# Kernel tuning notes

Hardware: AMD Instinct MI355X
Metric: run time of the kernel (lower is better)

## Reference

```python
import jax, jax.numpy as jnp
import numpy as np
import math

NL = 2
ENC = 64

def _ln(x, g, b):
    m = x.mean(-1, keepdims=True)
    v = ((x - m) ** 2).mean(-1, keepdims=True)
    return (x - m) * jax.lax.rsqrt(v + 1e-5) * g + b

def _sinu(vals):
    half = ENC // 2
    freq = jnp.exp(jnp.arange(half, dtype=vals.dtype) * (-math.log(10000.0) / half))
    a = vals[..., None] * freq
    return jnp.concatenate([jnp.sin(a), jnp.cos(a)], -1)

def _ssm(x, ng, nb, piw, pib, pw, pb, ig, ib):
    # SSMBlock with LinearAttention core: x + proj_out(LN(silu(z)*sigmoid(gate)))
    h = _ln(x, ng, nb)
    zi = h @ piw + pib
    z, gate = jnp.split(zi, 2, axis=-1)
    u = _ln(jax.nn.silu(z) * jax.nn.sigmoid(gate), ig, ib)
    return x + u @ pw + pb

def _fwd(s, attn_maps, km, se_w1, se_b1, se_w2, se_b2,
         f_ng, f_nb, f_piw, f_pib, f_pow, f_pob, f_ig, f_ib,
         b_ng, b_nb, b_piw, b_pib, b_pow, b_pob, b_ig, b_ib,
         mrg_w, mrg_b, nrm_g, nrm_b,
         ffn_ng, ffn_nb, ffn_w1, ffn_b1, ffn_w2, ffn_b2, H, W):
    B, K, D = s.shape
    w = attn_maps / (attn_maps.sum(-1, keepdims=True) + 1e-8)  # [B,K,N]
    gy = jnp.arange(H, dtype=s.dtype) / max(H - 1, 1)
    gx = jnp.arange(W, dtype=s.dtype) / max(W - 1, 1)
    grid_y = jnp.repeat(gy, W)  # [N], meshgrid-ij flattened
    grid_x = jnp.tile(gx, H)
    cy = (w * grid_y).sum(-1)  # [B,K]
    cx = (w * grid_x).sum(-1)
    spread = jnp.sqrt((w * ((grid_y - cy[..., None]) ** 2 + (grid_x - cx[..., None]) ** 2)).sum(-1))
    enc = jnp.concatenate([_sinu(cy), _sinu(cx), spread[..., None]], -1)  # [B,K,129]
    s = s + jax.nn.gelu(enc @ se_w1 + se_b1, approximate=False) @ se_w2 + se_b2
    # spatial order: identical every layer since attn_maps is fixed
    order = jnp.argsort(cy * W + cx, axis=-1)  # [B,K]
    rv = jnp.argsort(order, axis=-1)           # inverse permutation
    for i in range(NL):
        r = s
        so = jnp.take_along_axis(s, order[..., None], axis=1)
        f = _ssm(so, f_ng[i], f_nb[i], f_piw[i], f_pib[i], f_pow[i], f_pob[i], f_ig[i], f_ib[i])
        bb = jnp.flip(_ssm(jnp.flip(so, 1), b_ng[i], b_nb[i], b_piw[i], b_pib[i], b_pow[i], b_pob[i], b_ig[i], b_ib[i]), 1)
        m = jnp.concatenate([f, bb], -1) @ mrg_w[i] + mrg_b[i]
        s = _ln(r + jnp.take_along_axis(m, rv[..., None], axis=1), nrm_g[i], nrm_b[i])
        h = _ln(s, ffn_ng[i], ffn_nb[i])
        s = s + jax.nn.gelu(h @ ffn_w1[i] + ffn_b1[i], approximate=False) @ ffn_w2[i] + ffn_b2[i]
        s = s * km[..., None]
    return s

def setup_inputs() -> dict:
    B, K, D, DI, H, W = 32, 256, 512, 1024, 64, 64
    N = H * W
    ks = iter(jax.random.split(jax.random.key(0), 64))
    def g(shape, sc=0.02):
        return jax.random.normal(next(ks), shape, dtype=jnp.float32) * sc
    inp = {
        's': jax.random.normal(next(ks), (B, K, D), dtype=jnp.float32),
        'attn_maps': jax.random.uniform(next(ks), (B, K, N), dtype=jnp.float32),
        'km': jnp.ones((B, K), jnp.float32),
        'se_w1': g((2 * ENC + 1, D)), 'se_b1': jnp.zeros((D,), jnp.float32),
        'se_w2': g((D, D)), 'se_b2': jnp.zeros((D,), jnp.float32),
    }
    for p in ('f', 'b'):
        inp[p + '_ng'] = jnp.ones((NL, D), jnp.float32)
        inp[p + '_nb'] = jnp.zeros((NL, D), jnp.float32)
        inp[p + '_piw'] = g((NL, D, 2 * DI))
        inp[p + '_pib'] = jnp.zeros((NL, 2 * DI), jnp.float32)
        inp[p + '_pow'] = g((NL, DI, D))
        inp[p + '_pob'] = jnp.zeros((NL, D), jnp.float32)
        inp[p + '_ig'] = jnp.ones((NL, DI), jnp.float32)
        inp[p + '_ib'] = jnp.zeros((NL, DI), jnp.float32)
    inp['mrg_w'] = g((NL, 2 * D, D)); inp['mrg_b'] = jnp.zeros((NL, D), jnp.float32)
    inp['nrm_g'] = jnp.ones((NL, D), jnp.float32); inp['nrm_b'] = jnp.zeros((NL, D), jnp.float32)
    inp['ffn_ng'] = jnp.ones((NL, D), jnp.float32); inp['ffn_nb'] = jnp.zeros((NL, D), jnp.float32)
    inp['ffn_w1'] = g((NL, D, 4 * D)); inp['ffn_b1'] = jnp.zeros((NL, 4 * D), jnp.float32)
    inp['ffn_w2'] = g((NL, 4 * D, D)); inp['ffn_b2'] = jnp.zeros((NL, D), jnp.float32)
    inp['H'] = H
    inp['W'] = W
    return inp

def reference(s, attn_maps, km, se_w1, se_b1, se_w2, se_b2,
              f_ng, f_nb, f_piw, f_pib, f_pow, f_pob, f_ig, f_ib,
              b_ng, b_nb, b_piw, b_pib, b_pow, b_pob, b_ig, b_ib,
              mrg_w, mrg_b, nrm_g, nrm_b,
              ffn_ng, ffn_nb, ffn_w1, ffn_b1, ffn_w2, ffn_b2, H, W):
    return _fwd(s, attn_maps, km, se_w1, se_b1, se_w2, se_b2,
                f_ng, f_nb, f_piw, f_pib, f_pow, f_pob, f_ig, f_ib,
                b_ng, b_nb, b_piw, b_pib, b_pow, b_pob, b_ig, b_ib,
                mrg_w, mrg_b, nrm_g, nrm_b,
                ffn_ng, ffn_nb, ffn_w1, ffn_b1, ffn_w2, ffn_b2, H, W)
```

## Files before the change

### kernel.cpp

```cpp
#include <hip/hip_runtime.h>
#include <cstdint>
#include <cstddef>


typedef unsigned short u16;
typedef __bf16 bf16x8 __attribute__((ext_vector_type(8)));
typedef float f32x4 __attribute__((ext_vector_type(4)));

#define MROWS 8192

__device__ __forceinline__ u16 f2bf(float f){
  unsigned u = __float_as_uint(f);
  u += 0x7FFFu + ((u >> 16) & 1u);
  return (u16)(u >> 16);
}
__device__ __forceinline__ float bf2f(u16 v){
  return __uint_as_float((unsigned)v << 16);
}

__device__ __forceinline__ float wred64(float v){
#pragma unroll
  for (int o = 32; o > 0; o >>= 1) v += __shfl_xor(v, o, 64);
  return v;
}

#define GLD16(gp, lp) __builtin_amdgcn_global_load_lds( \
    (const __attribute__((address_space(1))) unsigned int*)(gp), \
    (__attribute__((address_space(3))) unsigned int*)(lp), 16, 0, 0)

struct TDesc { const float* src; u16* dst; int R, Kpad, C, zgate, nbx, base; };
struct TPack { TDesc d[16]; };

__global__ __launch_bounds__(256) void transpose_all(TPack p){
  int bid = blockIdx.x;
  TDesc dd = p.d[0];
#pragma unroll
  for (int i = 1; i < 16; ++i) if (bid >= p.d[i].base) dd = p.d[i];
  int lb = bid - dd.base;
  int bx = lb % dd.nbx, by = lb / dd.nbx;

  __shared__ float tile[32][33];
  int n0 = bx << 5, k0 = by << 5;
  int tx = threadIdx.x & 31, ty = threadIdx.x >> 5;
#pragma unroll
  for (int i = 0; i < 32; i += 8){
    int k = k0 + ty + i, n = n0 + tx;
    int oc = n;
    if (dd.zgate){ int g = n >> 5, sl = n & 31;
      oc = (sl < 16) ? (g << 4) + sl : (dd.C >> 1) + (g << 4) + sl - 16; }
    tile[ty + i][tx] = (k < dd.R) ? dd.src[(size_t)k * dd.C + oc] : 0.f;
  }
  __syncthreads();
#pragma unroll
  for (int i = 0; i < 32; i += 8){
    int n = n0 + ty + i, k = k0 + tx;
    dd.dst[(size_t)n * dd.Kpad + k] = f2bf(tile[tx][ty + i]);
  }
}

__global__ __launch_bounds__(256) void stats_enc(
    const float* __restrict__ attn, u16* __restrict__ enc){
  int row = blockIdx.x;
  const float4* a4 = (const float4*)(attn + (size_t)row * 4096);
  int t = threadIdx.x;
  const float inv63 = 1.0f / 63.0f;
  float s0 = 0, sy = 0, sx = 0, sy2 = 0, sx2 = 0;
#pragma unroll
  for (int i = 0; i < 4; ++i){
    int c = t + 256 * i;
    float4 v = a4[c];
    int n = 4 * c;
#pragma unroll
    for (int e = 0; e < 4; ++e){
      float av = (&v.x)[e];
      int nn = n + e;
      float gy = (float)(nn >> 6) * inv63;
      float gx = (float)(nn & 63) * inv63;
      s0 += av; sy += av * gy; sx += av * gx;
      sy2 += av * gy * gy; sx2 += av * gx * gx;
    }
  }
  s0 = wred64(s0); sy = wred64(sy); sx = wred64(sx);
  sy2 = wred64(sy2); sx2 = wred64(sx2);
  __shared__ float red[4][5];
  __shared__ float outv[3];
  int wv = t >> 6, lane = t & 63;
  if (lane == 0){ red[wv][0]=s0; red[wv][1]=sy; red[wv][2]=sx; red[wv][3]=sy2; red[wv][4]=sx2; }
  __syncthreads();
  if (t == 0){
    float S=0, Ay=0, Ax=0, Ay2=0, Ax2=0;
    for (int w = 0; w < 4; ++w){ S+=red[w][0]; Ay+=red[w][1]; Ax+=red[w][2]; Ay2+=red[w][3]; Ax2+=red[w][4]; }
    float denom = S + 1e-8f;
    float cy = Ay / denom, cx = Ax / denom;
    float sp2 = (Ay2 - 2.f*cy*Ay + cy*cy*S + Ax2 - 2.f*cx*Ax + cx*cx*S) / denom;
    outv[0] = cy; outv[1] = cx; outv[2] = sqrtf(fmaxf(sp2, 0.f));
  }
  __syncthreads();
  if (t < 192){
    float cy = outv[0], cx = outv[1];
    float val = 0.f;
    if (t < 128){
      int j = t & 31;
      float fr = expf(-0.28782313662425572f * (float)j);
      float base = (t < 64) ? cy : cx;
      float ang = base * fr;
      val = ((t >> 5) & 1) ? cosf(ang) : sinf(ang);
    } else if (t == 128) val = outv[2];
    enc[(size_t)row * 192 + t] = f2bf(val);
  }
}

__global__ __launch_bounds__(256) void ln_dual(
    const float* __restrict__ x,
    const float* __restrict__ g1, const float* __restrict__ b1,
    const float* __restrict__ g2, const float* __restrict__ b2,
    u16* __restrict__ o1, u16* __restrict__ o2){
  int row = blockIdx.x * 4 + (threadIdx.x >> 6);
  int lane = threadIdx.x & 63, c = lane * 8;
  const float* xr = x + (size_t)row * 512 + c;
  float v[8];
  *(float4*)(v) = *(const float4*)(xr); *(float4*)(v+4) = *(const float4*)(xr+4);
  float s = 0.f;
#pragma unroll
  for (int j = 0; j < 8; ++j) s += v[j];
  float m = wred64(s) * (1.f/512.f);
  float q = 0.f;
#pragma unroll
  for (int j = 0; j < 8; ++j){ float d = v[j]-m; q += d*d; }
  float rstd = rsqrtf(wred64(q)*(1.f/512.f) + 1e-5f);
  float G1[8],B1[8],G2[8],B2[8];
  *(float4*)(G1)=*(const float4*)(g1+c); *(float4*)(G1+4)=*(const float4*)(g1+c+4);
  *(float4*)(B1)=*(const float4*)(b1+c); *(float4*)(B1+4)=*(const float4*)(b1+c+4);
  *(float4*)(G2)=*(const float4*)(g2+c); *(float4*)(G2+4)=*(const float4*)(g2+c+4);
  *(float4*)(B2)=*(const float4*)(b2+c); *(float4*)(B2+4)=*(const float4*)(b2+c+4);
  u16 u1[8] __attribute__((aligned(16)));
  u16 u2[8] __attribute__((aligned(16)));
#pragma unroll
  for (int j = 0; j < 8; ++j){
    float nv = (v[j]-m)*rstd;
    u1[j] = f2bf(nv*G1[j]+B1[j]);
    u2[j] = f2bf(nv*G2[j]+B2[j]);
  }
  *(uint4*)(o1 + (size_t)row*512 + c) = *(const uint4*)u1;
  *(uint4*)(o2 + (size_t)row*512 + c) = *(const uint4*)u2;
}

__global__ __launch_bounds__(256) void ln1024(
    const u16* __restrict__ x,
    const float* __restrict__ gf, const float* __restrict__ bfp,
    const float* __restrict__ gb, const float* __restrict__ bbp,
    u16* __restrict__ o){
  int row = blockIdx.x * 4 + (threadIdx.x >> 6);
  int lane = threadIdx.x & 63, c = lane * 16;
  const float* g = (row >> 13) ? gb : gf;
  const float* b = (row >> 13) ? bbp : bfp;
  const u16* xr = x + (size_t)row * 1024 + c;
  u16 raw[16] __attribute__((aligned(16)));
  *(uint4*)(raw)     = *(const uint4*)(xr);
  *(uint4*)(raw + 8) = *(const uint4*)(xr + 8);
  float v[16];
#pragma unroll
  for (int j = 0; j < 16; ++j) v[j] = bf2f(raw[j]);
  float s = 0.f;
#pragma unroll
  for (int j = 0; j < 16; ++j) s += v[j];
  float m = wred64(s) * (1.f/1024.f);
  float q = 0.f;
#pragma unroll
  for (int j = 0; j < 16; ++j){ float d = v[j]-m; q += d*d; }
  float rstd = rsqrtf(wred64(q)*(1.f/1024.f) + 1e-5f);
  float G[16], B[16];
#pragma unroll
  for (int i = 0; i < 4; ++i){
    *(float4*)(G + 4*i) = *(const float4*)(g + c + 4*i);
    *(float4*)(B + 4*i) = *(const float4*)(b + c + 4*i);
  }
  u16 u[16] __attribute__((aligned(16)));
#pragma unroll
  for (int j = 0; j < 16; ++j) u[j] = f2bf((v[j]-m)*rstd*G[j] + B[j]);
  *(uint4*)(o + (size_t)row*1024 + c)     = *(const uint4*)(u);
  *(uint4*)(o + (size_t)row*1024 + c + 8) = *(const uint4*)(u + 8);
}

__global__ __launch_bounds__(256) void ln_double(
    const u16* __restrict__ x,
    const float* __restrict__ ng, const float* __restrict__ nb,
    const float* __restrict__ fg, const float* __restrict__ fbv,
    u16* __restrict__ s1, u16* __restrict__ h2){
  int row = blockIdx.x * 4 + (threadIdx.x >> 6);
  int lane = threadIdx.x & 63, c = lane * 8;
  const u16* xr = x + (size_t)row * 512 + c;
  u16 raw[8] __attribute__((aligned(16)));
  *(uint4*)(raw) = *(const uint4*)(xr);
  float v[8];
#pragma unroll
  for (int j = 0; j < 8; ++j) v[j] = bf2f(raw[j]);
  float s = 0.f;
#pragma unroll
  for (int j = 0; j < 8; ++j) s += v[j];
  float m = wred64(s) * (1.f/512.f);
  float q = 0.f;
#pragma unroll
  for (int j = 0; j < 8; ++j){ float d = v[j]-m; q += d*d; }
  float rstd = rsqrtf(wred64(q)*(1.f/512.f) + 1e-5f);
  float NG[8],NB[8],FG[8],FB[8];
  *(float4*)(NG)=*(const float4*)(ng+c); *(float4*)(NG+4)=*(const float4*)(ng+c+4);
  *(float4*)(NB)=*(const float4*)(nb+c); *(float4*)(NB+4)=*(const float4*)(nb+c+4);
  *(float4*)(FG)=*(const float4*)(fg+c); *(float4*)(FG+4)=*(const float4*)(fg+c+4);
  *(float4*)(FB)=*(const float4*)(fbv+c);*(float4*)(FB+4)=*(const float4*)(fbv+c+4);
  float w[8];
#pragma unroll
  for (int j = 0; j < 8; ++j) w[j] = (v[j]-m)*rstd*NG[j] + NB[j];
  u16 us[8] __attribute__((aligned(16)));
#pragma unroll
  for (int j = 0; j < 8; ++j) us[j] = f2bf(w[j]);
  *(uint4*)(s1 + (size_t)row*512 + c) = *(const uint4*)us;
  float s2 = 0.f;
#pragma unroll
  for (int j = 0; j < 8; ++j) s2 += w[j];
  float m2 = wred64(s2) * (1.f/512.f);
  float q2 = 0.f;
#pragma unroll
  for (int j = 0; j < 8; ++j){ float d = w[j]-m2; q2 += d*d; }
  float rstd2 = rsqrtf(wred64(q2)*(1.f/512.f) + 1e-5f);
  u16 u[8] __attribute__((aligned(16)));
#pragma unroll
  for (int j = 0; j < 8; ++j) u[j] = f2bf((w[j]-m2)*rstd2*FG[j] + FB[j]);
  *(uint4*)(h2 + (size_t)row*512 + c) = *(const uint4*)u;
}

template<int EPI, int BM>
__global__ __launch_bounds__(256, (BM == 64) ? 4 : 2) void gemm_bt(
    const u16* __restrict__ A,
    const u16* __restrict__ BT0, const u16* __restrict__ BT1,
    const float* __restrict__ bias0, const float* __restrict__ bias1,
    const void* __restrict__ res,
    float* __restrict__ outF, u16* __restrict__ outB,
    const float* __restrict__ km,
    int K, int N, int ldo){
  constexpr int MR = BM / 32;
  __shared__ u16 Asm[BM * 64];
  __shared__ u16 Bsm[128 * 64];
  const int tid = threadIdx.x, wv = tid >> 6, lane = tid & 63;
  const int m0 = blockIdx.y * BM, n0 = blockIdx.x << 7;
  const int wr = wv >> 1, wc = wv & 1;
  const u16* BT = (m0 < MROWS) ? BT0 : BT1;
  const float* bias = (m0 < MROWS) ? bias0 : bias1;

  const int rowin = lane >> 3;
  const int ksrc = ((16 * (lane & 7)) ^ (rowin << 4)) >> 1;
  const int rA = wv * (BM / 4) + rowin;
  const int rB = (wv << 5) + rowin;
  const u16* gA = A + (size_t)(m0 + rA) * K + ksrc;
  const u16* gB = BT + (size_t)(n0 + rB) * K + ksrc;
  u16* ldsA = Asm + wv * (BM / 4) * 64;
  u16* ldsB = Bsm + (wv << 11);

  f32x4 acc[MR][4] = {};
  const int cbase = 16 * (lane >> 4);
  const int swz = (lane & 7) << 4;

  for (int kt = 0; kt < K; kt += 64){
#pragma unroll
    for (int it = 0; it < BM / 32; ++it)
      GLD16(gA + (size_t)it * 8 * K + kt, ldsA + it * 512);
#pragma unroll
    for (int it = 0; it < 4; ++it)
      GLD16(gB + (size_t)it * 8 * K + kt, ldsB + it * 512);
    __syncthreads();
#pragma unroll
    for (int ks = 0; ks < 64; ks += 32){
      const int cs = ((2 * ks + cbase) ^ swz) >> 1;
      bf16x8 af[MR], bfr[4];
#pragma unroll
      for (int m = 0; m < MR; ++m)
        af[m] = *reinterpret_cast<const bf16x8*>(&Asm[(wr*(BM/2) + m*16 + (lane & 15)) * 64 + cs]);
#pragma unroll
      for (int n = 0; n < 4; ++n)
        bfr[n] = *reinterpret_cast<const bf16x8*>(&Bsm[(wc*64 + n*16 + (lane & 15)) * 64 + cs]);
#pragma unroll
      for (int m = 0; m < MR; ++m)
#pragma unroll
        for (int n = 0; n < 4; ++n)
          acc[m][n] = __builtin_amdgcn_mfma_f32_16x16x32_bf16(af[m], bfr[n], acc[m][n], 0, 0, 0);
    }
    __syncthreads();
  }

  const int lr = (lane >> 4) << 2, lc = lane & 15;
#pragma unroll
  for (int m = 0; m < MR; ++m){
    const int grow0 = m0 + wr * (BM/2) + m * 16 + lr;
    if constexpr (EPI == 3){
#pragma unroll
      for (int n = 0; n < 4; n += 2){
        const int zc = n0 + wc * 64 + n * 16 + lc;
        const int bi = ((zc >> 5) << 4) + lc;
        const float bz = bias[bi], bg = bias[(N >> 1) + bi];
        const int ucol = ((n0 + wc * 64) >> 1) + (n << 3) + lc;
#pragma unroll
        for (int r = 0; r < 4; ++r){
          float z = acc[m][n][r] + bz;
          float g = acc[m][n + 1][r] + bg;
          outB[(size_t)(grow0 + r) * ldo + ucol] =
              f2bf((z / (1.f + expf(-z))) * (1.f / (1.f + expf(-g))));
        }
      }
    } else {
#pragma unroll
      for (int n = 0; n < 4; ++n){
        const int col = n0 + wc * 64 + n * 16 + lc;
        const float bv = bias[col];
#pragma unroll
        for (int r = 0; r < 4; ++r){
          const int grow = grow0 + r;
          float v = acc[m][n][r] + bv;
          if constexpr (EPI == 0){
            outB[(size_t)grow * ldo + col] = f2bf(0.5f * v * (1.f + erff(v * 0.70710678118654752f)));
          } else if constexpr (EPI == 1){
            outF[(size_t)grow * ldo + col] = v + ((const float*)res)[(size_t)grow * N + col];
          } else if constexpr (EPI == 2){
            outF[(size_t)grow * ldo + col] =
                (v + bf2f(((const u16*)res)[(size_t)grow * N + col])) * km[grow];
          } else {
            const int rowout = grow & (MROWS - 1);
            const int coloff = (grow >> 13) << 9;
            outB[(size_t)rowout * ldo + coloff + col] =
                f2bf(v + ((const float*)res)[(size_t)rowout * N + col]);
          }
        }
      }
    }
  }
}

extern "C" void kernel_launch(void* const* d_in, const int* in_sizes, int n_in,
                              void* d_out, int out_size, void* d_ws, size_t ws_size,
                              hipStream_t stream){
  (void)in_sizes; (void)n_in; (void)out_size; (void)ws_size;
  const float* s_in   = (const float*)d_in[0];
  const float* attn   = (const float*)d_in[1];
  const float* km     = (const float*)d_in[2];
  const float* se_w1  = (const float*)d_in[3];
  const float* se_b1  = (const float*)d_in[4];
  const float* se_w2  = (const float*)d_in[5];
  const float* se_b2  = (const float*)d_in[6];
  const float* png[2] = {(const float*)d_in[7],  (const float*)d_in[15]};
  const float* pnb[2] = {(const float*)d_in[8],  (const float*)d_in[16]};
  const float* ppiw[2]= {(const float*)d_in[9],  (const float*)d_in[17]};
  const float* ppib[2]= {(const float*)d_in[10], (const float*)d_in[18]};
  const float* ppow[2]= {(const float*)d_in[11], (const float*)d_in[19]};
  const float* ppob[2]= {(const float*)d_in[12], (const float*)d_in[20]};
  const float* pig[2] = {(const float*)d_in[13], (const float*)d_in[21]};
  const float* pibt[2]= {(const float*)d_in[14], (const float*)d_in[22]};
  const float* mrg_w  = (const float*)d_in[23];
  const float* mrg_b  = (const float*)d_in[24];
  const float* nrm_g  = (const float*)d_in[25];
  const float* nrm_b  = (const float*)d_in[26];
  const float* ffn_ng = (const float*)d_in[27];
  const float* ffn_nb = (const float*)d_in[28];
  const float* ffn_w1 = (const float*)d_in[29];
  const float* ffn_b1 = (const float*)d_in[30];
  const float* ffn_w2 = (const float*)d_in[31];
  const float* ffn_b2 = (const float*)d_in[32];
  float* out = (float*)d_out;

  char* ws = (char*)d_ws;
  size_t off = 0;
  auto alloc = [&](size_t bytes)->char*{
    char* p = ws + off; off += (bytes + 255) & ~(size_t)255; return p; };

  u16* w_sew1 = (u16*)alloc(512 * 192 * 2);
  u16* w_sew2 = (u16*)alloc(512 * 512 * 2);
  u16* w_piw[2][2]; u16* w_pow[2][2];
  for (int d = 0; d < 2; ++d)
    for (int i = 0; i < 2; ++i){
      w_piw[d][i] = (u16*)alloc(2048 * 512 * 2);
      w_pow[d][i] = (u16*)alloc(512 * 1024 * 2);
    }
  u16* w_mrg[2]; u16* w_ffn1[2]; u16* w_ffn2[2];
  for (int i = 0; i < 2; ++i){
    w_mrg[i]  = (u16*)alloc(512 * 1024 * 2);
    w_ffn1[i] = (u16*)alloc(2048 * 512 * 2);
    w_ffn2[i] = (u16*)alloc(512 * 2048 * 2);
  }
  u16*   enc  = (u16*)alloc((size_t)MROWS * 192 * 2);
  u16*   t1h2 = (u16*)alloc((size_t)MROWS * 512 * 2);
  float* sc   = (float*)alloc((size_t)MROWS * 512 * 4);
  u16*   hcat = (u16*)alloc((size_t)2 * MROWS * 512 * 2);
  char*  big  = alloc((size_t)MROWS * 2048 * 2);
  u16*   upre = (u16*)big;
  u16*   r2   = (u16*)big;
  u16*   t2   = (u16*)big;
  u16*   ubf  = (u16*)alloc((size_t)2 * MROWS * 1024 * 2);
  u16*   fbuf = (u16*)alloc((size_t)MROWS * 1024 * 2);
  u16*   s1   = (u16*)alloc((size_t)MROWS * 512 * 2);

  TPack pk; int base = 0, di = 0;
  auto push = [&](const float* src, u16* dst, int R, int Kpad, int C, int zg){
    TDesc& t = pk.d[di++];
    t.src = src; t.dst = dst; t.R = R; t.Kpad = Kpad; t.C = C; t.zgate = zg;
    t.nbx = C / 32; t.base = base;
    base += (C / 32) * (Kpad / 32);
  };
  push(se_w1, w_sew1, 129, 192, 512, 0);
  push(se_w2, w_sew2, 512, 512, 512, 0);
  for (int d = 0; d < 2; ++d)
    for (int i = 0; i < 2; ++i){
      push(ppiw[d] + (size_t)i*512*2048, w_piw[d][i], 512, 512, 2048, 1);
      push(ppow[d] + (size_t)i*1024*512, w_pow[d][i], 1024, 1024, 512, 0);
    }
  for (int i = 0; i < 2; ++i){
    push(mrg_w  + (size_t)i*1024*512, w_mrg[i],  1024, 1024, 512, 0);
    push(ffn_w1 + (size_t)i*512*2048, w_ffn1[i], 512, 512, 2048, 0);
    push(ffn_w2 + (size_t)i*2048*512, w_ffn2[i], 2048, 2048, 512, 0);
  }
  transpose_all<<<base, 256, 0, stream>>>(pk);

  stats_enc<<<MROWS, 256, 0, stream>>>(attn, enc);
  gemm_bt<0,64><<<dim3(4, 128), 256, 0, stream>>>(enc, w_sew1, w_sew1, se_b1, se_b1,
      nullptr, nullptr, t1h2, nullptr, 192, 512, 512);
  gemm_bt<1,64><<<dim3(4, 128), 256, 0, stream>>>(t1h2, w_sew2, w_sew2, se_b2, se_b2,
      s_in, sc, nullptr, nullptr, 512, 512, 512);

  for (int i = 0; i < 2; ++i){
    ln_dual<<<MROWS/4, 256, 0, stream>>>(sc, png[0]+i*512, pnb[0]+i*512,
        png[1]+i*512, pnb[1]+i*512, hcat, hcat + (size_t)MROWS*512);
    gemm_bt<3,128><<<dim3(16, 128), 256, 0, stream>>>(hcat,
        w_piw[0][i], w_piw[1][i], ppib[0]+(size_t)i*2048, ppib[1]+(size_t)i*2048,
        nullptr, nullptr, upre, nullptr, 512, 2048, 1024);
    ln1024<<<(2*MROWS)/4, 256, 0, stream>>>(upre,
        pig[0]+i*1024, pibt[0]+i*1024, pig[1]+i*1024, pibt[1]+i*1024, ubf);
    gemm_bt<4,64><<<dim3(4, 256), 256, 0, stream>>>(ubf,
        w_pow[0][i], w_pow[1][i], ppob[0]+i*512, ppob[1]+i*512,
        sc, nullptr, fbuf, nullptr, 1024, 512, 1024);
    gemm_bt<4,64><<<dim3(4, 128), 256, 0, stream>>>(fbuf,
        w_mrg[i], w_mrg[i], mrg_b+i*512, mrg_b+i*512,
        sc, nullptr, r2, nullptr, 1024, 512, 512);
    ln_double<<<MROWS/4, 256, 0, stream>>>(r2, nrm_g+i*512, nrm_b+i*512,
        ffn_ng+i*512, ffn_nb+i*512, s1, t1h2);
    gemm_bt<0,128><<<dim3(16, 64), 256, 0, stream>>>(t1h2,
        w_ffn1[i], w_ffn1[i], ffn_b1+i*2048, ffn_b1+i*2048,
        nullptr, nullptr, t2, nullptr, 512, 2048, 2048);
    gemm_bt<2,64><<<dim3(4, 128), 256, 0, stream>>>(t2,
        w_ffn2[i], w_ffn2[i], ffn_b2+i*512, ffn_b2+i*512,
        s1, (i == 1 ? out : sc), nullptr, km, 2048, 512, 512);
  }
}
```

Before: 751.9 us.

## Add 256x256 tile GEMM with phased LDS double-buffering for wide projections

Adds a new gemm256 kernel that uses 512 threads, 256x256 output tiles, 128KB of swizzled LDS with two buffers, and an interleaved schedule. In that schedule, global-to-LDS loads for the next K tiles are issued between MFMA phases, with explicit waitcnt, barriers and setprio. It replaces the gemm_bt calls for the SSM input projection (gate epilogue) and the FFN first layer (GELU epilogue). Blocks are remapped in groups of eight to improve L2 locality. The goal is more data reuse per tile and better overlap of memory traffic with matrix cores, at the cost of a single workgroup per CU and fewer blocks (256 for FFN1).

```diff
diff --git a/kernel.cpp b/kernel.cpp
--- a/kernel.cpp
+++ b/kernel.cpp
@@ -27,6 +27,11 @@
 #define GLD16(gp, lp) __builtin_amdgcn_global_load_lds( \
     (const __attribute__((address_space(1))) unsigned int*)(gp), \
     (__attribute__((address_space(3))) unsigned int*)(lp), 16, 0, 0)
+
+#define BARRIER() do { asm volatile("" ::: "memory"); \
+  __builtin_amdgcn_s_barrier(); asm volatile("" ::: "memory"); } while(0)
+#define VMW(n) asm volatile("s_waitcnt vmcnt(" #n ")" ::: "memory")
+#define LGKM0() asm volatile("s_waitcnt lgkmcnt(0)" ::: "memory")
 
 struct TDesc { const float* src; u16* dst; int R, Kpad, C, zgate, nbx, base; };
 struct TPack { TDesc d[16]; };
@@ -291,13 +296,163 @@
 #pragma unroll
   for (int m = 0; m < MR; ++m){
     const int grow0 = m0 + wr * (BM/2) + m * 16 + lr;
+#pragma unroll
+    for (int n = 0; n < 4; ++n){
+      const int col = n0 + wc * 64 + n * 16 + lc;
+      const float bv = bias[col];
+#pragma unroll
+      for (int r = 0; r < 4; ++r){
+        const int grow = grow0 + r;
+        float v = acc[m][n][r] + bv;
+        if constexpr (EPI == 0){
+          outB[(size_t)grow * ldo + col] = f2bf(0.5f * v * (1.f + erff(v * 0.70710678118654752f)));
+        } else if constexpr (EPI == 1){
+          outF[(size_t)grow * ldo + col] = v + ((const float*)res)[(size_t)grow * N + col];
+        } else if constexpr (EPI == 2){
+          outF[(size_t)grow * ldo + col] =
+              (v + bf2f(((const u16*)res)[(size_t)grow * N + col])) * km[grow];
+        } else {
+          const int rowout = grow & (MROWS - 1);
+          const int coloff = (grow >> 13) << 9;
+          outB[(size_t)rowout * ldo + coloff + col] =
+              f2bf(v + ((const float*)res)[(size_t)rowout * N + col]);
+        }
+      }
+    }
+  }
+}
+
+template<int EPI>
+__global__ __launch_bounds__(512, 1) void gemm256(
+    const u16* __restrict__ A,
+    const u16* __restrict__ BT0, const u16* __restrict__ BT1,
+    const float* __restrict__ bias0, const float* __restrict__ bias1,
+    u16* __restrict__ outB, int K, int N, int ldo, int nwg){
+  extern __shared__ u16 lds[];
+  const int tid = threadIdx.x, w = tid >> 6, lane = tid & 63;
+  int bid = (blockIdx.x & 7) * (nwg >> 3) + (blockIdx.x >> 3);
+  const int nbx = N >> 8;
+  const int m0 = (bid / nbx) << 8, n0 = (bid % nbx) << 8;
+  const u16* BT = (m0 < MROWS) ? BT0 : BT1;
+  const float* bias = (m0 < MROWS) ? bias0 : bias1;
+  const int wm = w >> 2, wn = w & 3;
+
+  const int srow = (w << 3) + (lane >> 3);
+  const int scol = ((16 * (lane & 7)) ^ (((lane >> 3) & 7) << 4)) >> 1;
+  const u16* gA = A + (size_t)(m0 + srow) * K + scol;
+  const u16* gB = BT + (size_t)(n0 + srow) * K + scol;
+  const int dstw = (w << 3) * 64;
+
+  auto stA = [&](int b, int h, int kt){
+    const u16* s = gA + (size_t)(h << 7) * K + (kt << 6);
+    u16* d = &lds[((b << 1) + 0) * 16384 + (h << 7) * 64 + dstw];
+    GLD16(s, d); GLD16(s + (size_t)64 * K, d + 64 * 64);
+  };
+  auto stB = [&](int b, int h, int kt){
+    const u16* s = gB + (size_t)(h << 7) * K + (kt << 6);
+    u16* d = &lds[((b << 1) + 1) * 16384 + (h << 7) * 64 + dstw];
+    GLD16(s, d); GLD16(s + (size_t)64 * K, d + 64 * 64);
+  };
+
+  const int swz = (lane & 7) << 4;
+  const int cb = (lane >> 4) << 4;
+  const int fr = lane & 15;
+  auto ldA = [&](int b, int mf, int ks)->bf16x8 {
+    int row = (wm << 7) + (mf << 4) + fr;
+    int byte = ((ks << 6) + cb) ^ swz;
+    return *reinterpret_cast<const bf16x8*>(&lds[((b << 1) + 0) * 16384 + row * 64 + (byte >> 1)]);
+  };
+  auto ldB = [&](int b, int nf, int ks)->bf16x8 {
+    int row = (wn << 6) + (nf << 4) + fr;
+    int byte = ((ks << 6) + cb) ^ swz;
+    return *reinterpret_cast<const bf16x8*>(&lds[((b << 1) + 1) * 16384 + row * 64 + (byte >> 1)]);
+  };
+
+  f32x4 acc[8][4] = {};
+  bf16x8 aA[8], bB[2][4];
+  const int nt2 = K >> 7;
+
+  stA(0,0,0); stA(0,1,0); stB(0,0,0); stB(0,1,0);
+  stB(1,0,1); stB(1,1,1);
+  VMW(4);
+  BARRIER();
+
+#pragma unroll 1
+  for (int j = 0; j < nt2; ++j){
+    const int kt1 = 2*j + 1;
+    const bool more = (j + 1 < nt2);
+    const int ktn0 = 2*j + 2, ktn1 = 2*j + 3;
+
+#define PHASE_MFMA(MB, BH)                                              \
+    BARRIER(); LGKM0();                                                 \
+    __builtin_amdgcn_s_setprio(1);                                      \
+    _Pragma("unroll")                                                   \
+    for (int m = 0; m < 4; ++m)                                         \
+      _Pragma("unroll")                                                 \
+      for (int n = 0; n < 2; ++n){                                      \
+        acc[(MB)*4+m][(BH)*2+n] = __builtin_amdgcn_mfma_f32_16x16x32_bf16( \
+            aA[2*m],   bB[BH][2*n],   acc[(MB)*4+m][(BH)*2+n], 0,0,0);  \
+        acc[(MB)*4+m][(BH)*2+n] = __builtin_amdgcn_mfma_f32_16x16x32_bf16( \
+            aA[2*m+1], bB[BH][2*n+1], acc[(MB)*4+m][(BH)*2+n], 0,0,0);  \
+      }                                                                 \
+    __builtin_amdgcn_s_setprio(0)
+
+#pragma unroll
+    for (int m = 0; m < 4; ++m){ aA[2*m] = ldA(0,m,0); aA[2*m+1] = ldA(0,m,1); }
+#pragma unroll
+    for (int n = 0; n < 2; ++n){ bB[0][2*n] = ldB(0,n,0); bB[0][2*n+1] = ldB(0,n,1); }
+    stA(1,0,kt1);
+    PHASE_MFMA(0,0);
+    BARRIER();
+#pragma unroll
+    for (int n = 0; n < 2; ++n){ bB[1][2*n] = ldB(0,n+2,0); bB[1][2*n+1] = ldB(0,n+2,1); }
+    stA(1,1,kt1);
+    PHASE_MFMA(0,1);
+    BARRIER();
+#pragma unroll
+    for (int m = 0; m < 4; ++m){ aA[2*m] = ldA(0,m+4,0); aA[2*m+1] = ldA(0,m+4,1); }
+    if (more) stB(0,0,ktn0);
+    PHASE_MFMA(1,1);
+    BARRIER();
+    if (more) stB(0,1,ktn0);
+    PHASE_MFMA(1,0);
+    if (more) { VMW(4); } else { VMW(0); }
+    BARRIER();
+#pragma unroll
+    for (int m = 0; m < 4; ++m){ aA[2*m] = ldA(1,m,0); aA[2*m+1] = ldA(1,m,1); }
+#pragma unroll
+    for (int n = 0; n < 2; ++n){ bB[0][2*n] = ldB(1,n,0); bB[0][2*n+1] = ldB(1,n,1); }
+    if (more) stA(0,0,ktn0);
+    PHASE_MFMA(0,0);
+    BARRIER();
+#pragma unroll
+    for (int n = 0; n < 2; ++n){ bB[1][2*n] = ldB(1,n+2,0); bB[1][2*n+1] = ldB(1,n+2,1); }
+    if (more) stA(0,1,ktn0);
+    PHASE_MFMA(0,1);
+    BARRIER();
+#pragma unroll
+    for (int m = 0; m < 4; ++m){ aA[2*m] = ldA(1,m+4,0); aA[2*m+1] = ldA(1,m+4,1); }
+    if (more) stB(1,0,ktn1);
+    PHASE_MFMA(1,1);
+    BARRIER();
+    if (more) stB(1,1,ktn1);
+    PHASE_MFMA(1,0);
+    VMW(4);
+    BARRIER();
+#undef PHASE_MFMA
+  }
+
+  const int lr = (lane >> 4) << 2, lc = lane & 15;
+#pragma unroll
+  for (int m = 0; m < 8; ++m){
+    const int grow0 = m0 + (wm << 7) + m * 16 + lr;
     if constexpr (EPI == 3){
 #pragma unroll
       for (int n = 0; n < 4; n += 2){
-        const int zc = n0 + wc * 64 + n * 16 + lc;
+        const int zc = n0 + (wn << 6) + n * 16 + lc;
         const int bi = ((zc >> 5) << 4) + lc;
         const float bz = bias[bi], bg = bias[(N >> 1) + bi];
-        const int ucol = ((n0 + wc * 64) >> 1) + (n << 3) + lc;
+        const int ucol = ((n0 + (wn << 6)) >> 1) + (n << 3) + lc;
 #pragma unroll
         for (int r = 0; r < 4; ++r){
           float z = acc[m][n][r] + bz;
@@ -309,25 +464,13 @@
     } else {
 #pragma unroll
       for (int n = 0; n < 4; ++n){
-        const int col = n0 + wc * 64 + n * 16 + lc;
+        const int col = n0 + (wn << 6) + n * 16 + lc;
         const float bv = bias[col];
 #pragma unroll
         for (int r = 0; r < 4; ++r){
-          const int grow = grow0 + r;
           float v = acc[m][n][r] + bv;
-          if constexpr (EPI == 0){
-            outB[(size_t)grow * ldo + col] = f2bf(0.5f * v * (1.f + erff(v * 0.70710678118654752f)));
-          } else if constexpr (EPI == 1){
-            outF[(size_t)grow * ldo + col] = v + ((const float*)res)[(size_t)grow * N + col];
-          } else if constexpr (EPI == 2){
-            outF[(size_t)grow * ldo + col] =
-                (v + bf2f(((const u16*)res)[(size_t)grow * N + col])) * km[grow];
-          } else {
-            const int rowout = grow & (MROWS - 1);
-            const int coloff = (grow >> 13) << 9;
-            outB[(size_t)rowout * ldo + coloff + col] =
-                f2bf(v + ((const float*)res)[(size_t)rowout * N + col]);
-          }
+          outB[(size_t)(grow0 + r) * ldo + col] =
+              f2bf(0.5f * v * (1.f + erff(v * 0.70710678118654752f)));
         }
       }
     }
@@ -426,9 +569,9 @@
   for (int i = 0; i < 2; ++i){
     ln_dual<<<MROWS/4, 256, 0, stream>>>(sc, png[0]+i*512, pnb[0]+i*512,
         png[1]+i*512, pnb[1]+i*512, hcat, hcat + (size_t)MROWS*512);
-    gemm_bt<3,128><<<dim3(16, 128), 256, 0, stream>>>(hcat,
+    gemm256<3><<<512, 512, 131072, stream>>>(hcat,
         w_piw[0][i], w_piw[1][i], ppib[0]+(size_t)i*2048, ppib[1]+(size_t)i*2048,
-        nullptr, nullptr, upre, nullptr, 512, 2048, 1024);
+        upre, 512, 2048, 1024, 512);
     ln1024<<<(2*MROWS)/4, 256, 0, stream>>>(upre,
         pig[0]+i*1024, pibt[0]+i*1024, pig[1]+i*1024, pibt[1]+i*1024, ubf);
     gemm_bt<4,64><<<dim3(4, 256), 256, 0, stream>>>(ubf,
@@ -439,9 +582,9 @@
         sc, nullptr, r2, nullptr, 1024, 512, 512);
     ln_double<<<MROWS/4, 256, 0, stream>>>(r2, nrm_g+i*512, nrm_b+i*512,
         ffn_ng+i*512, ffn_nb+i*512, s1, t1h2);
-    gemm_bt<0,128><<<dim3(16, 64), 256, 0, stream>>>(t1h2,
+    gemm256<0><<<256, 512, 131072, stream>>>(t1h2,
         w_ffn1[i], w_ffn1[i], ffn_b1+i*2048, ffn_b1+i*2048,
-        nullptr, nullptr, t2, nullptr, 512, 2048, 2048);
+        t2, 512, 2048, 2048, 256);
     gemm_bt<2,64><<<dim3(4, 128), 256, 0, stream>>>(t2,
         w_ffn2[i], w_ffn2[i], ffn_b2+i*512, ffn_b2+i*512,
         s1, (i == 1 ? out : sc), nullptr, km, 2048, 512, 512);
```

Result: slower. 788.3 us (+4.8%).

## Fold SSM input LayerNorm affine into in-proj weights and merge directions into one GEMM

Applied to the files above, without the earlier changes.

Folds the forward and backward LayerNorm gamma into the transposed in-projection weights, and folds beta times W into a precomputed bias. A single normalized activation is then shared by both directions. The two directional in-proj GEMMs over stacked rows become one GEMM with N=4096, reading A once instead of twice, and ln_dual shrinks to a plain normalize. Downstream kernels now use strided A and interleaved output layouts. The cost is an extra bias-fold kernel and some change in bf16 rounding, since gamma is applied before weight quantization.

```diff
diff --git a/kernel.cpp b/kernel.cpp
--- a/kernel.cpp
+++ b/kernel.cpp
@@ -28,7 +28,8 @@
     (const __attribute__((address_space(1))) unsigned int*)(gp), \
     (__attribute__((address_space(3))) unsigned int*)(lp), 16, 0, 0)
 
-struct TDesc { const float* src; u16* dst; int R, Kpad, C, zgate, nbx, base; };
+struct TDesc { const float* src; u16* dst; const float* scl;
+               int R, Kpad, C, zgate, nbx, base; };
 struct TPack { TDesc d[16]; };
 
 __global__ __launch_bounds__(256) void transpose_all(TPack p){
@@ -48,7 +49,12 @@
     int oc = n;
     if (dd.zgate){ int g = n >> 5, sl = n & 31;
       oc = (sl < 16) ? (g << 4) + sl : (dd.C >> 1) + (g << 4) + sl - 16; }
-    tile[ty + i][tx] = (k < dd.R) ? dd.src[(size_t)k * dd.C + oc] : 0.f;
+    float val = 0.f;
+    if (k < dd.R){
+      val = dd.src[(size_t)k * dd.C + oc];
+      if (dd.scl) val *= dd.scl[k];
+    }
+    tile[ty + i][tx] = val;
   }
   __syncthreads();
 #pragma unroll
@@ -56,6 +62,21 @@
     int n = n0 + ty + i, k = k0 + tx;
     dd.dst[(size_t)n * dd.Kpad + k] = f2bf(tile[tx][ty + i]);
   }
+}
+
+__global__ __launch_bounds__(256) void bias_fold(
+    const float* __restrict__ pib0, const float* __restrict__ pib1,
+    const float* __restrict__ pnb0, const float* __restrict__ pnb1,
+    const float* __restrict__ piw0, const float* __restrict__ piw1,
+    float* __restrict__ outb){
+  int c = blockIdx.x >> 3, d = c >> 1, i = c & 1;
+  int n = ((blockIdx.x & 7) << 8) + threadIdx.x;
+  const float* pib = (d ? pib1 : pib0) + (size_t)i * 2048;
+  const float* nb  = (d ? pnb1 : pnb0) + (size_t)i * 512;
+  const float* W   = (d ? piw1 : piw0) + (size_t)i * 512 * 2048;
+  float a = pib[n];
+  for (int k = 0; k < 512; ++k) a += nb[k] * W[(size_t)k * 2048 + n];
+  outb[(size_t)c * 2048 + n] = a;
 }
 
 __global__ __launch_bounds__(256) void stats_enc(
@@ -110,11 +131,8 @@
   }
 }
 
-__global__ __launch_bounds__(256) void ln_dual(
-    const float* __restrict__ x,
-    const float* __restrict__ g1, const float* __restrict__ b1,
-    const float* __restrict__ g2, const float* __restrict__ b2,
-    u16* __restrict__ o1, u16* __restrict__ o2){
+__global__ __launch_bounds__(256) void ln_norm(
+    const float* __restrict__ x, u16* __restrict__ o){
   int row = blockIdx.x * 4 + (threadIdx.x >> 6);
   int lane = threadIdx.x & 63, c = lane * 8;
   const float* xr = x + (size_t)row * 512 + c;
@@ -128,21 +146,10 @@
 #pragma unroll
   for (int j = 0; j < 8; ++j){ float d = v[j]-m; q += d*d; }
   float rstd = rsqrtf(wred64(q)*(1.f/512.f) + 1e-5f);
-  float G1[8],B1[8],G2[8],B2[8];
-  *(float4*)(G1)=*(const float4*)(g1+c); *(float4*)(G1+4)=*(const float4*)(g1+c+4);
-  *(float4*)(B1)=*(const float4*)(b1+c); *(float4*)(B1+4)=*(const float4*)(b1+c+4);
-  *(float4*)(G2)=*(const float4*)(g2+c); *(float4*)(G2+4)=*(const float4*)(g2+c+4);
-  *(float4*)(B2)=*(const float4*)(b2+c); *(float4*)(B2+4)=*(const float4*)(b2+c+4);
   u16 u1[8] __attribute__((aligned(16)));
-  u16 u2[8] __attribute__((aligned(16)));
-#pragma unroll
-  for (int j = 0; j < 8; ++j){
-    float nv = (v[j]-m)*rstd;
-    u1[j] = f2bf(nv*G1[j]+B1[j]);
-    u2[j] = f2bf(nv*G2[j]+B2[j]);
-  }
-  *(uint4*)(o1 + (size_t)row*512 + c) = *(const uint4*)u1;
-  *(uint4*)(o2 + (size_t)row*512 + c) = *(const uint4*)u2;
+#pragma unroll
+  for (int j = 0; j < 8; ++j) u1[j] = f2bf((v[j]-m)*rstd);
+  *(uint4*)(o + (size_t)row*512 + c) = *(const uint4*)u1;
 }
 
 __global__ __launch_bounds__(256) void ln1024(
@@ -150,14 +157,15 @@
     const float* __restrict__ gf, const float* __restrict__ bfp,
     const float* __restrict__ gb, const float* __restrict__ bbp,
     u16* __restrict__ o){
-  int row = blockIdx.x * 4 + (threadIdx.x >> 6);
+  int vr = blockIdx.x * 4 + (threadIdx.x >> 6);
+  int row = vr >> 1, half = vr & 1;
   int lane = threadIdx.x & 63, c = lane * 16;
-  const float* g = (row >> 13) ? gb : gf;
-  const float* b = (row >> 13) ? bbp : bfp;
-  const u16* xr = x + (size_t)row * 1024 + c;
+  const float* g = half ? gb : gf;
+  const float* b = half ? bbp : bfp;
+  size_t base = (size_t)row * 2048 + half * 1024 + c;
   u16 raw[16] __attribute__((aligned(16)));
-  *(uint4*)(raw)     = *(const uint4*)(xr);
-  *(uint4*)(raw + 8) = *(const uint4*)(xr + 8);
+  *(uint4*)(raw)     = *(const uint4*)(x + base);
+  *(uint4*)(raw + 8) = *(const uint4*)(x + base + 8);
   float v[16];
 #pragma unroll
   for (int j = 0; j < 16; ++j) v[j] = bf2f(raw[j]);
@@ -178,8 +186,8 @@
   u16 u[16] __attribute__((aligned(16)));
 #pragma unroll
   for (int j = 0; j < 16; ++j) u[j] = f2bf((v[j]-m)*rstd*G[j] + B[j]);
-  *(uint4*)(o + (size_t)row*1024 + c)     = *(const uint4*)(u);
-  *(uint4*)(o + (size_t)row*1024 + c + 8) = *(const uint4*)(u + 8);
+  *(uint4*)(o + base)     = *(const uint4*)(u);
+  *(uint4*)(o + base + 8) = *(const uint4*)(u + 8);
 }
 
 __global__ __launch_bounds__(256) void ln_double(
@@ -231,7 +239,7 @@
 
 template<int EPI, int BM>
 __global__ __launch_bounds__(256, (BM == 64) ? 4 : 2) void gemm_bt(
-    const u16* __restrict__ A,
+    const u16* __restrict__ A0, const u16* __restrict__ A1, int lda,
     const u16* __restrict__ BT0, const u16* __restrict__ BT1,
     const float* __restrict__ bias0, const float* __restrict__ bias1,
     const void* __restrict__ res,
@@ -244,14 +252,16 @@
   const int tid = threadIdx.x, wv = tid >> 6, lane = tid & 63;
   const int m0 = blockIdx.y * BM, n0 = blockIdx.x << 7;
   const int wr = wv >> 1, wc = wv & 1;
+  const u16* A = (m0 < MROWS) ? A0 : A1;
   const u16* BT = (m0 < MROWS) ? BT0 : BT1;
   const float* bias = (m0 < MROWS) ? bias0 : bias1;
+  const int mbase = m0 & (MROWS - 1);
 
   const int rowin = lane >> 3;
   const int ksrc = ((16 * (lane & 7)) ^ (rowin << 4)) >> 1;
   const int rA = wv * (BM / 4) + rowin;
   const int rB = (wv << 5) + rowin;
-  const u16* gA = A + (size_t)(m0 + rA) * K + ksrc;
+  const u16* gA = A + (size_t)(mbase + rA) * lda + ksrc;
   const u16* gB = BT + (size_t)(n0 + rB) * K + ksrc;
   u16* ldsA = Asm + wv * (BM / 4) * 64;
   u16* ldsB = Bsm + (wv << 11);
@@ -263,7 +273,7 @@
   for (int kt = 0; kt < K; kt += 64){
 #pragma unroll
     for (int it = 0; it < BM / 32; ++it)
-      GLD16(gA + (size_t)it * 8 * K + kt, ldsA + it * 512);
+      GLD16(gA + (size_t)it * 8 * lda + kt, ldsA + it * 512);
 #pragma unroll
     for (int it = 0; it < 4; ++it)
       GLD16(gB + (size_t)it * 8 * K + kt, ldsB + it * 512);
@@ -295,9 +305,12 @@
 #pragma unroll
       for (int n = 0; n < 4; n += 2){
         const int zc = n0 + wc * 64 + n * 16 + lc;
-        const int bi = ((zc >> 5) << 4) + lc;
-        const float bz = bias[bi], bg = bias[(N >> 1) + bi];
-        const int ucol = ((n0 + wc * 64) >> 1) + (n << 3) + lc;
+        const int dsel = zc >> 11;
+        const int loc = zc & 2047;
+        const int bi = ((loc >> 5) << 4) + lc;
+        const float* bz_p = dsel ? bias1 : bias0;
+        const float bz = bz_p[bi], bg = bz_p[1024 + bi];
+        const int ucol = (dsel << 10) + bi;
 #pragma unroll
         for (int r = 0; r < 4; ++r){
           float z = acc[m][n][r] + bz;
@@ -372,77 +385,81 @@
 
   u16* w_sew1 = (u16*)alloc(512 * 192 * 2);
   u16* w_sew2 = (u16*)alloc(512 * 512 * 2);
-  u16* w_piw[2][2]; u16* w_pow[2][2];
+  u16* w_piwC[2]; u16* w_pow[2][2];
+  for (int i = 0; i < 2; ++i) w_piwC[i] = (u16*)alloc((size_t)4096 * 512 * 2);
   for (int d = 0; d < 2; ++d)
-    for (int i = 0; i < 2; ++i){
-      w_piw[d][i] = (u16*)alloc(2048 * 512 * 2);
+    for (int i = 0; i < 2; ++i)
       w_pow[d][i] = (u16*)alloc(512 * 1024 * 2);
-    }
   u16* w_mrg[2]; u16* w_ffn1[2]; u16* w_ffn2[2];
   for (int i = 0; i < 2; ++i){
     w_mrg[i]  = (u16*)alloc(512 * 1024 * 2);
     w_ffn1[i] = (u16*)alloc(2048 * 512 * 2);
     w_ffn2[i] = (u16*)alloc(512 * 2048 * 2);
   }
+  float* pibC = (float*)alloc((size_t)4 * 2048 * 4);
   u16*   enc  = (u16*)alloc((size_t)MROWS * 192 * 2);
   u16*   t1h2 = (u16*)alloc((size_t)MROWS * 512 * 2);
   float* sc   = (float*)alloc((size_t)MROWS * 512 * 4);
-  u16*   hcat = (u16*)alloc((size_t)2 * MROWS * 512 * 2);
+  u16*   hnv  = (u16*)alloc((size_t)MROWS * 512 * 2);
   char*  big  = alloc((size_t)MROWS * 2048 * 2);
-  u16*   upre = (u16*)big;
+  u16*   u    = (u16*)big;
   u16*   r2   = (u16*)big;
   u16*   t2   = (u16*)big;
-  u16*   ubf  = (u16*)alloc((size_t)2 * MROWS * 1024 * 2);
+  u16*   ubf  = (u16*)alloc((size_t)MROWS * 2048 * 2);
   u16*   fbuf = (u16*)alloc((size_t)MROWS * 1024 * 2);
   u16*   s1   = (u16*)alloc((size_t)MROWS * 512 * 2);
 
   TPack pk; int base = 0, di = 0;
-  auto push = [&](const float* src, u16* dst, int R, int Kpad, int C, int zg){
+  auto push = [&](const float* src, u16* dst, int R, int Kpad, int C, int zg,
+                  const float* scl){
     TDesc& t = pk.d[di++];
-    t.src = src; t.dst = dst; t.R = R; t.Kpad = Kpad; t.C = C; t.zgate = zg;
+    t.src = src; t.dst = dst; t.scl = scl;
+    t.R = R; t.Kpad = Kpad; t.C = C; t.zgate = zg;
     t.nbx = C / 32; t.base = base;
     base += (C / 32) * (Kpad / 32);
   };
-  push(se_w1, w_sew1, 129, 192, 512, 0);
-  push(se_w2, w_sew2, 512, 512, 512, 0);
-  for (int d = 0; d < 2; ++d)
-    for (int i = 0; i < 2; ++i){
-      push(ppiw[d] + (size_t)i*512*2048, w_piw[d][i], 512, 512, 2048, 1);
-      push(ppow[d] + (size_t)i*1024*512, w_pow[d][i], 1024, 1024, 512, 0);
+  push(se_w1, w_sew1, 129, 192, 512, 0, nullptr);
+  push(se_w2, w_sew2, 512, 512, 512, 0, nullptr);
+  for (int i = 0; i < 2; ++i)
+    for (int d = 0; d < 2; ++d){
+      push(ppiw[d] + (size_t)i*512*2048, w_piwC[i] + (size_t)d*2048*512,
+           512, 512, 2048, 1, png[d] + i*512);
+      push(ppow[d] + (size_t)i*1024*512, w_pow[d][i], 1024, 1024, 512, 0, nullptr);
     }
   for (int i = 0; i < 2; ++i){
-    push(mrg_w  + (size_t)i*1024*512, w_mrg[i],  1024, 1024, 512, 0);
-    push(ffn_w1 + (size_t)i*512*2048, w_ffn1[i], 512, 512, 2048, 0);
-    push(ffn_w2 + (size_t)i*2048*512, w_ffn2[i], 2048, 2048, 512, 0);
+    push(mrg_w  + (size_t)i*1024*512, w_mrg[i],  1024, 1024, 512, 0, nullptr);
+    push(ffn_w1 + (size_t)i*512*2048, w_ffn1[i], 512, 512, 2048, 0, nullptr);
+    push(ffn_w2 + (size_t)i*2048*512, w_ffn2[i], 2048, 2048, 512, 0, nullptr);
   }
   transpose_all<<<base, 256, 0, stream>>>(pk);
+  bias_fold<<<32, 256, 0, stream>>>(ppib[0], ppib[1], pnb[0], pnb[1],
+                                    ppiw[0], ppiw[1], pibC);
 
   stats_enc<<<MROWS, 256, 0, stream>>>(attn, enc);
-  gemm_bt<0,64><<<dim3(4, 128), 256, 0, stream>>>(enc, w_sew1, w_sew1, se_b1, se_b1,
-      nullptr, nullptr, t1h2, nullptr, 192, 512, 512);
-  gemm_bt<1,64><<<dim3(4, 128), 256, 0, stream>>>(t1h2, w_sew2, w_sew2, se_b2, se_b2,
-      s_in, sc, nullptr, nullptr, 512, 512, 512);
+  gemm_bt<0,64><<<dim3(4, 128), 256, 0, stream>>>(enc, enc, 192,
+      w_sew1, w_sew1, se_b1, se_b1, nullptr, nullptr, t1h2, nullptr, 192, 512, 512);
+  gemm_bt<1,64><<<dim3(4, 128), 256, 0, stream>>>(t1h2, t1h2, 512,
+      w_sew2, w_sew2, se_b2, se_b2, s_in, sc, nullptr, nullptr, 512, 512, 512);
 
   for (int i = 0; i < 2; ++i){
-    ln_dual<<<MROWS/4, 256, 0, stream>>>(sc, png[0]+i*512, pnb[0]+i*512,
-        png[1]+i*512, pnb[1]+i*512, hcat, hcat + (size_t)MROWS*512);
-    gemm_bt<3,128><<<dim3(16, 128), 256, 0, stream>>>(hcat,
-        w_piw[0][i], w_piw[1][i], ppib[0]+(size_t)i*2048, ppib[1]+(size_t)i*2048,
-        nullptr, nullptr, upre, nullptr, 512, 2048, 1024);
-    ln1024<<<(2*MROWS)/4, 256, 0, stream>>>(upre,
+    ln_norm<<<MROWS/4, 256, 0, stream>>>(sc, hnv);
+    gemm_bt<3,128><<<dim3(32, 64), 256, 0, stream>>>(hnv, hnv, 512,
+        w_piwC[i], w_piwC[i], pibC + (size_t)i*2048, pibC + (size_t)(2+i)*2048,
+        nullptr, nullptr, u, nullptr, 512, 4096, 2048);
+    ln1024<<<(2*MROWS)/4, 256, 0, stream>>>(u,
         pig[0]+i*1024, pibt[0]+i*1024, pig[1]+i*1024, pibt[1]+i*1024, ubf);
-    gemm_bt<4,64><<<dim3(4, 256), 256, 0, stream>>>(ubf,
+    gemm_bt<4,64><<<dim3(4, 256), 256, 0, stream>>>(ubf, ubf + 1024, 2048,
         w_pow[0][i], w_pow[1][i], ppob[0]+i*512, ppob[1]+i*512,
         sc, nullptr, fbuf, nullptr, 1024, 512, 1024);
-    gemm_bt<4,64><<<dim3(4, 128), 256, 0, stream>>>(fbuf,
+    gemm_bt<4,64><<<dim3(4, 128), 256, 0, stream>>>(fbuf, fbuf, 1024,
         w_mrg[i], w_mrg[i], mrg_b+i*512, mrg_b+i*512,
         sc, nullptr, r2, nullptr, 1024, 512, 512);
     ln_double<<<MROWS/4, 256, 0, stream>>>(r2, nrm_g+i*512, nrm_b+i*512,
         ffn_ng+i*512, ffn_nb+i*512, s1, t1h2);
-    gemm_bt<0,128><<<dim3(16, 64), 256, 0, stream>>>(t1h2,
+    gemm_bt<0,128><<<dim3(16, 64), 256, 0, stream>>>(t1h2, t1h2, 512,
         w_ffn1[i], w_ffn1[i], ffn_b1+i*2048, ffn_b1+i*2048,
         nullptr, nullptr, t2, nullptr, 512, 2048, 2048);
-    gemm_bt<2,64><<<dim3(4, 128), 256, 0, stream>>>(t2,
+    gemm_bt<2,64><<<dim3(4, 128), 256, 0, stream>>>(t2, t2, 2048,
         w_ffn2[i], w_ffn2[i], ffn_b2+i*512, ffn_b2+i*512,
         s1, (i == 1 ? out : sc), nullptr, km, 2048, 512, 512);
   }
```

Result: slower. 827.1 us (+10.0%).
